# Kernel optimization log

Hardware: AMD Instinct MI355X
Metric: run time of the kernel (lower is better)

The kernel has to match this reference:

```python
import jax, jax.numpy as jnp
import numpy as np
from jax import lax

BS = 256
EPS = 1e-5  # torch LayerNorm default


def _layernorm(x, g, b):
    m = jnp.mean(x, axis=-1, keepdims=True)
    v = jnp.var(x, axis=-1, keepdims=True)
    return (x - m) / jnp.sqrt(v + EPS) * g + b


def _conv(x, w, b):
    y = lax.conv_general_dilated(x, w, (1, 1), 'VALID',
                                 dimension_numbers=('NCHW', 'OIHW', 'NCHW'))
    return y + b[None, :, None, None]


def _maxpool2(x):
    return lax.reduce_window(x, -jnp.inf, lax.max, (1, 1, 2, 2), (1, 1, 2, 2), 'VALID')


def setup_inputs() -> dict:
    key = jax.random.key(0)
    ks = iter(jax.random.split(key, 64))
    def rn(shape, scale=0.05):
        return jax.random.normal(next(ks), shape, dtype=jnp.float32) * scale
    return dict(
        t=jax.random.uniform(next(ks), (BS, 128, 128), dtype=jnp.float32) * 255.0,
        conv1_w=rn((32, 1, 3, 3)), conv1_b=rn((32,)),
        conv2_w=rn((32, 32, 3, 3)), conv2_b=rn((32,)),
        exp_w=rn((36, 64)), exp_b=rn((64,)),
        # 16 tile-attention modules x 4 heads x (64 -> 16)
        mh_wq=rn((16, 4, 64, 16)), mh_bq=rn((16, 4, 16)),
        mh_wk=rn((16, 4, 64, 16)), mh_bk=rn((16, 4, 16)),
        mh_wv=rn((16, 4, 64, 16)), mh_bv=rn((16, 4, 16)),
        mh_wo=rn((16, 64, 64)), mh_bo=rn((16, 64)),
        ln1_g=jnp.ones((64,), jnp.float32), ln1_b=jnp.zeros((64,), jnp.float32),
        # 2 XL layers x 8 heads x (2048 -> 256)
        xl_wq=rn((2, 8, 2048, 256)), xl_bq=rn((2, 8, 256)),
        xl_wk=rn((2, 8, 2048, 256)), xl_bk=rn((2, 8, 256)),
        xl_wv=rn((2, 8, 2048, 256)), xl_bv=rn((2, 8, 256)),
        xl_wo=rn((2, 2048, 2048)), xl_bo=rn((2, 2048)),
        xln_g=jnp.ones((2, 2048), jnp.float32), xln_b=jnp.zeros((2, 2048), jnp.float32),
        fl1_w=rn((32768, 512)), fl1_b=rn((512,)),
        fl2_w=rn((512, 128)), fl2_b=rn((128,)),
        fl3_w=rn((128, 25)), fl3_b=rn((25,)),
    )


def reference(t, conv1_w, conv1_b, conv2_w, conv2_b, exp_w, exp_b,
              mh_wq, mh_bq, mh_wk, mh_bk, mh_wv, mh_bv, mh_wo, mh_bo,
              ln1_g, ln1_b,
              xl_wq, xl_bq, xl_wk, xl_bk, xl_wv, xl_bv, xl_wo, xl_bo,
              xln_g, xln_b, fl1_w, fl1_b, fl2_w, fl2_b, fl3_w, fl3_b):
    # Eval-mode forward with discard_mem=True (fresh KV memory): every
    # AttentionHead attends over the current step only; dropout = identity.
    bs = t.shape[0]
    x = t / 255.0
    # 4x4 tiling of 32x32 patches -> (bs*16, 1, 32, 32)
    sliced = x.reshape(bs, 4, 32, 4, 32).transpose(0, 1, 3, 2, 4)
    x = sliced.reshape(bs * 16, 1, 32, 32)
    u = _maxpool2(_conv(x, conv1_w, conv1_b))        # (bs*16, 32, 15, 15)
    u = _maxpool2(_conv(u, conv2_w, conv2_b))        # (bs*16, 32, 6, 6)
    u = u.reshape(bs * 16, 32, 36)
    u = jax.nn.relu(u @ exp_w + exp_b)               # (bs*16, 32, 64)
    u = u.reshape(16, bs, 32, 64)                    # raw reshape, as in source

    # 16 multihead modules, 4 heads each, d_feature=16, seq_len=32
    q = jnp.einsum('mbsd,mhdf->mbhsf', u, mh_wq) + mh_bq[:, None, :, None, :]
    k = jnp.einsum('mbsd,mhdf->mbhsf', u, mh_wk) + mh_bk[:, None, :, None, :]
    v = jnp.einsum('mbsd,mhdf->mbhsf', u, mh_wv) + mh_bv[:, None, :, None, :]
    a = jax.nn.softmax(jnp.einsum('mbhsf,mbhtf->mbhst', q, k) / jnp.sqrt(16.0), axis=-1)
    o = jnp.einsum('mbhst,mbhtf->mbhsf', a, v)
    o = o.transpose(0, 1, 3, 2, 4).reshape(16, bs, 32, 64)  # concat heads
    o = jnp.einsum('mbsd,mde->mbse', o, mh_wo) + mh_bo[:, None, None, :]
    u = _layernorm(u + o, ln1_g, ln1_b)
    u = u.reshape(16, bs, 2048).transpose(1, 0, 2)   # (bs, 16, 2048)

    # XL stage (as written in source: att output is computed but discarded,
    # u = u + dropout(u) -> 2u under identity dropout, then LayerNorm)
    for i in range(2):
        q = jnp.einsum('bsd,hdf->bhsf', u, xl_wq[i]) + xl_bq[i][None, :, None, :]
        k = jnp.einsum('bsd,hdf->bhsf', u, xl_wk[i]) + xl_bk[i][None, :, None, :]
        vv = jnp.einsum('bsd,hdf->bhsf', u, xl_wv[i]) + xl_bv[i][None, :, None, :]
        aw = jax.nn.softmax(jnp.einsum('bhsf,bhtf->bhst', q, k) / jnp.sqrt(256.0), axis=-1)
        oo = jnp.einsum('bhst,bhtf->bhsf', aw, vv).transpose(0, 2, 1, 3).reshape(bs, 16, 2048)
        oo = oo @ xl_wo[i] + xl_bo[i]  # discarded, matching the source
        u = u + u
        u = _layernorm(u, xln_g[i], xln_b[i])

    u = u.reshape(bs, 16 * 2048)
    u = jax.nn.relu(u @ fl1_w + fl1_b)
    u = jax.nn.relu(u @ fl2_w + fl2_b)
    return u @ fl3_w + fl3_b
```

## Files before the change

kernel.cpp:

```cpp
#include <hip/hip_runtime.h>
#include <hip/hip_bf16.h>
#include <math.h>

#define LN_EPS 1e-5f

typedef __attribute__((ext_vector_type(8))) short short8v;
typedef __attribute__((ext_vector_type(4))) float f32x4;

static __device__ __forceinline__ unsigned short f2bf(float x) {
    unsigned u = __float_as_uint(x);
    u += 0x7fffu + ((u >> 16) & 1u);
    return (unsigned short)(u >> 16);
}
static __device__ __forceinline__ float bf2f(unsigned short h) {
    return __uint_as_float(((unsigned)h) << 16);
}

#define MFMA3(ACC, AH, AL, BH, BL)                                          \
    ACC = __builtin_amdgcn_mfma_f32_16x16x32_bf16(AH, BH, ACC, 0, 0, 0);    \
    ACC = __builtin_amdgcn_mfma_f32_16x16x32_bf16(AL, BH, ACC, 0, 0, 0);    \
    ACC = __builtin_amdgcn_mfma_f32_16x16x32_bf16(AH, BL, ACC, 0, 0, 0);

__global__ __launch_bounds__(512, 4) void k_conv(
    const float* __restrict__ t,
    const float* __restrict__ c1w, const float* __restrict__ c1b,
    const float* __restrict__ c2w, const float* __restrict__ c2b,
    const float* __restrict__ ew,  const float* __restrict__ eb,
    float* __restrict__ u)
{
    __shared__ __align__(16) unsigned short s_W2[2][32 * 296];
    __shared__ __align__(16) unsigned short s_p1h[225 * 40];
    __shared__ __align__(16) unsigned short s_p1l[225 * 40];
    __shared__ __align__(16) float s_s2[32 * 36];
    __shared__ float s_c2b[32];

    float* s_x  = (float*)s_W2;
    float* s_ew = (float*)s_p1h;
    unsigned short* s_wh = s_W2[0];
    unsigned short* s_wl = s_W2[1];

    const int p   = blockIdx.x;
    const int tid = threadIdx.x;

    const int b = p >> 4, tile = p & 15, tr = tile >> 2, tc = tile & 3;
    const float* tp = t + (size_t)b * 128 * 128 + (size_t)tr * 32 * 128 + tc * 32;
    for (int i = tid; i < 1024; i += 512) {
        const int r = i >> 5, c = i & 31;
        s_x[r * 33 + c] = tp[r * 128 + c] * (1.0f / 255.0f);
    }
    if (tid < 32) s_c2b[tid] = c2b[tid];
    __syncthreads();

    if (tid < 450) {
        const int pos  = tid >> 1;
        const int half = tid & 1;
        const int pi = pos / 15, pj = pos % 15;
        float xw[16];
        #pragma unroll
        for (int r = 0; r < 4; ++r)
            #pragma unroll
            for (int c = 0; c < 4; ++c)
                xw[r * 4 + c] = s_x[(2 * pi + r) * 33 + (2 * pj + c)];
        #pragma unroll
        for (int og2 = 0; og2 < 2; ++og2) {
            const int og = half * 2 + og2;
            short8v hb, lb;
            #pragma unroll
            for (int o = 0; o < 8; ++o) {
                const int oc = og * 8 + o;
                float w[9];
                #pragma unroll
                for (int j = 0; j < 9; ++j) w[j] = c1w[oc * 9 + j];
                float mx = -3.0e38f;
                #pragma unroll
                for (int a = 0; a < 2; ++a)
                    #pragma unroll
                    for (int bb = 0; bb < 2; ++bb) {
                        float s = xw[(a + 0) * 4 + bb + 0] * w[0]
                                + xw[(a + 0) * 4 + bb + 1] * w[1]
                                + xw[(a + 0) * 4 + bb + 2] * w[2]
                                + xw[(a + 1) * 4 + bb + 0] * w[3]
                                + xw[(a + 1) * 4 + bb + 1] * w[4]
                                + xw[(a + 1) * 4 + bb + 2] * w[5]
                                + xw[(a + 2) * 4 + bb + 0] * w[6]
                                + xw[(a + 2) * 4 + bb + 1] * w[7]
                                + xw[(a + 2) * 4 + bb + 2] * w[8];
                        mx = fmaxf(mx, s);
                    }
                const float val = mx + c1b[oc];
                const unsigned short h = f2bf(val);
                hb[o] = (short)h;
                lb[o] = (short)f2bf(val - bf2f(h));
            }
            *(short8v*)&s_p1h[pos * 40 + og * 8] = hb;
            *(short8v*)&s_p1l[pos * 40 + og * 8] = lb;
        }
    }
    __syncthreads();

    {
        const int oc  = tid >> 4;
        const int sub = tid & 15;
        const float* wp = c2w + oc * 288 + sub * 18;
        float wf[18];
        #pragma unroll
        for (int j = 0; j < 9; ++j)
            *(float2*)&wf[j * 2] = *(const float2*)&wp[j * 2];
        #pragma unroll
        for (int ks = 0; ks < 9; ++ks) {
            const float v0 = wf[ks];
            const float v1 = wf[9 + ks];
            const unsigned short h0 = f2bf(v0), h1 = f2bf(v1);
            const unsigned short l0 = f2bf(v0 - bf2f(h0));
            const unsigned short l1 = f2bf(v1 - bf2f(h1));
            const int idx = oc * 296 + ks * 32 + sub * 2;
            *(unsigned*)&s_wh[idx] = (unsigned)h0 | ((unsigned)h1 << 16);
            *(unsigned*)&s_wl[idx] = (unsigned)l0 | ((unsigned)l1 << 16);
        }
    }
    __syncthreads();

    {
        const int lane = tid & 63;
        const int w8   = tid >> 6;
        const int jcol = lane & 15;
        const int icg8 = (lane >> 4) * 8;

        {
            const int nt = w8;
            const int n = nt * 16 + jcol;
            const int pq = n >> 2, w4 = n & 3;
            const int pi = pq / 6, pj = pq - pi * 6;
            const int rbase = 2 * pi + (w4 >> 1);
            const int cbase = 2 * pj + (w4 & 1);

            f32x4 acc0 = {0,0,0,0}, acc1 = {0,0,0,0};
            #pragma unroll
            for (int ks = 0; ks < 9; ++ks) {
                const int dr = ks / 3, dc = ks - dr * 3;
                const int ab = jcol * 296 + ks * 32 + icg8;
                const short8v ah0 = *(const short8v*)&s_wh[ab];
                const short8v ah1 = *(const short8v*)&s_wh[ab + 16 * 296];
                const short8v al0 = *(const short8v*)&s_wl[ab];
                const short8v al1 = *(const short8v*)&s_wl[ab + 16 * 296];
                const int boff = ((rbase + dr) * 15 + (cbase + dc)) * 40 + icg8;
                const short8v bh = *(const short8v*)&s_p1h[boff];
                const short8v bl = *(const short8v*)&s_p1l[boff];
                acc0 = __builtin_amdgcn_mfma_f32_16x16x32_bf16(ah0, bh, acc0, 0, 0, 0);
                acc0 = __builtin_amdgcn_mfma_f32_16x16x32_bf16(al0, bh, acc0, 0, 0, 0);
                acc0 = __builtin_amdgcn_mfma_f32_16x16x32_bf16(ah0, bl, acc0, 0, 0, 0);
                acc1 = __builtin_amdgcn_mfma_f32_16x16x32_bf16(ah1, bh, acc1, 0, 0, 0);
                acc1 = __builtin_amdgcn_mfma_f32_16x16x32_bf16(al1, bh, acc1, 0, 0, 0);
                acc1 = __builtin_amdgcn_mfma_f32_16x16x32_bf16(ah1, bl, acc1, 0, 0, 0);
            }
            #pragma unroll
            for (int mt = 0; mt < 2; ++mt)
                #pragma unroll
                for (int r = 0; r < 4; ++r) {
                    float v = (mt == 0) ? acc0[r] : acc1[r];
                    v = fmaxf(v, __shfl_xor(v, 1));
                    v = fmaxf(v, __shfl_xor(v, 2));
                    if ((lane & 3) == 0) {
                        const int oc = mt * 16 + (lane >> 4) * 4 + r;
                        const int pq2 = nt * 4 + (jcol >> 2);
                        s_s2[oc * 36 + pq2] = v + s_c2b[oc];
                    }
                }
        }

        if (w8 < 2) {
            const int nt = 8;
            const int mt = w8;
            const int n = nt * 16 + jcol;
            const int pq = n >> 2, w4 = n & 3;
            const int pi = pq / 6, pj = pq - pi * 6;
            const int rbase = 2 * pi + (w4 >> 1);
            const int cbase = 2 * pj + (w4 & 1);

            f32x4 accX = {0,0,0,0};
            #pragma unroll
            for (int ks = 0; ks < 9; ++ks) {
                const int dr = ks / 3, dc = ks - dr * 3;
                const int ab = jcol * 296 + ks * 32 + icg8 + mt * 16 * 296;
                const short8v ah = *(const short8v*)&s_wh[ab];
                const short8v al = *(const short8v*)&s_wl[ab];
                const int boff = ((rbase + dr) * 15 + (cbase + dc)) * 40 + icg8;
                const short8v bh = *(const short8v*)&s_p1h[boff];
                const short8v bl = *(const short8v*)&s_p1l[boff];
                accX = __builtin_amdgcn_mfma_f32_16x16x32_bf16(ah, bh, accX, 0, 0, 0);
                accX = __builtin_amdgcn_mfma_f32_16x16x32_bf16(al, bh, accX, 0, 0, 0);
                accX = __builtin_amdgcn_mfma_f32_16x16x32_bf16(ah, bl, accX, 0, 0, 0);
            }
            #pragma unroll
            for (int r = 0; r < 4; ++r) {
                float v = accX[r];
                v = fmaxf(v, __shfl_xor(v, 1));
                v = fmaxf(v, __shfl_xor(v, 2));
                if ((lane & 3) == 0) {
                    const int oc = mt * 16 + (lane >> 4) * 4 + r;
                    const int pq2 = nt * 4 + (jcol >> 2);
                    s_s2[oc * 36 + pq2] = v + s_c2b[oc];
                }
            }
        }
    }
    __syncthreads();

    for (int i = tid; i < 576; i += 512)
        *(float4*)&s_ew[i * 4] = *(const float4*)&ew[i * 4];
    __syncthreads();

    {
        const int s  = tid >> 4;
        const int e0 = (tid & 15) * 4;
        float acc4[4];
        *(float4*)&acc4[0] = *(const float4*)&eb[e0];
        for (int f = 0; f < 36; ++f) {
            const float sv = s_s2[s * 36 + f];
            const float4 w0 = *(const float4*)&s_ew[f * 64 + e0];
            acc4[0] += sv * w0.x; acc4[1] += sv * w0.y;
            acc4[2] += sv * w0.z; acc4[3] += sv * w0.w;
        }
        float4 o0;
        o0.x = fmaxf(acc4[0], 0.0f); o0.y = fmaxf(acc4[1], 0.0f);
        o0.z = fmaxf(acc4[2], 0.0f); o0.w = fmaxf(acc4[3], 0.0f);
        *(float4*)&u[(size_t)p * 2048 + s * 64 + e0] = o0;
    }
}

__global__ __launch_bounds__(256, 2) void k_attn(
    const float* __restrict__ u,
    const float* __restrict__ wq, const float* __restrict__ bq,
    const float* __restrict__ wk, const float* __restrict__ bk,
    const float* __restrict__ wv, const float* __restrict__ bv,
    const float* __restrict__ wo, const float* __restrict__ bo,
    const float* __restrict__ g1, const float* __restrict__ b1,
    const float* __restrict__ xg, const float* __restrict__ xb,
    unsigned short* __restrict__ Ah, unsigned short* __restrict__ Al)
{
    __shared__ __align__(16) unsigned short s_w[2][64 * 64];
    __shared__ __align__(16) float s_uf[32 * 68];
    __shared__ __align__(16) unsigned short R1[12288];
    __shared__ __align__(16) unsigned short R2[5632];
    __shared__ float s_red[2][32][2];
    __shared__ float s_red2[2][4][2];

    unsigned short* qA_h = R1;
    unsigned short* qA_l = R1 + 3072;
    unsigned short* kB_h = R1 + 6144;
    unsigned short* kB_l = R1 + 9216;
    unsigned short* p_h  = R1;
    unsigned short* p_l  = R1 + 5120;
    unsigned short* vT_h = R2;
    unsigned short* vT_l = R2 + 2560;
    unsigned short* oA_h = R2;
    unsigned short* oA_l = R2 + 2816;

    const int g   = blockIdx.x;
    const int m   = g >> 8;
    const int b2  = g & 255;
    const int tid = threadIdx.x;
    const int l   = tid & 63;
    const int w   = tid >> 6;
    const int l15 = l & 15;
    const int lg  = l >> 4;

    {
        const int s = tid >> 3, dq = (tid & 7) * 8;
        const float* up = u + (size_t)g * 2048 + s * 64 + dq;
        *(float4*)&s_uf[s * 68 + dq]     = *(const float4*)up;
        *(float4*)&s_uf[s * 68 + dq + 4] = *(const float4*)(up + 4);
    }

    const int wn  = tid & 63;
    const int wkq = tid >> 6;
    float wreg[16];

    #define LOADQKV(SRC)                                                          \
        {                                                                         \
            const float* sp = (SRC) + (size_t)m * 4096 + (wn >> 4) * 1024 + (wn & 15); \
            _Pragma("unroll")                                                     \
            for (int j = 0; j < 16; ++j) wreg[j] = sp[(wkq * 16 + j) * 16];       \
        }
    #define LOADO(SRC)                                                            \
        {                                                                         \
            const float* sp = (SRC) + (size_t)m * 4096 + wn;                      \
            _Pragma("unroll")                                                     \
            for (int j = 0; j < 16; ++j) wreg[j] = sp[(wkq * 16 + j) * 64];       \
        }
    #define WRITEW()                                                              \
        {                                                                         \
            _Pragma("unroll")                                                     \
            for (int j2 = 0; j2 < 8; ++j2) {                                      \
                const int d = wkq * 16 + j2 * 2;                                  \
                const float v0 = wreg[j2 * 2], v1 = wreg[j2 * 2 + 1];             \
                const unsigned short h0 = f2bf(v0), h1 = f2bf(v1);                \
                const unsigned short q0 = f2bf(v0 - bf2f(h0));                    \
                const unsigned short q1 = f2bf(v1 - bf2f(h1));                    \
                const int idx = wn * 64 + (((d >> 3) ^ (wn & 7)) << 3) + (d & 7); \
                *(unsigned*)&s_w[0][idx] = (unsigned)h0 | ((unsigned)h1 << 16);   \
                *(unsigned*)&s_w[1][idx] = (unsigned)q0 | ((unsigned)q1 << 16);   \
            }                                                                     \
        }

    LOADQKV(wq);
    __syncthreads();
    WRITEW();

    short8v uh[2][2], ul[2][2];
    #pragma unroll
    for (int mf = 0; mf < 2; ++mf)
        #pragma unroll
        for (int ks = 0; ks < 2; ++ks) {
            const float* pb = &s_uf[(mf * 16 + l15) * 68 + (ks * 4 + lg) * 8];
            float xv[8];
            *(float4*)&xv[0] = *(const float4*)pb;
            *(float4*)&xv[4] = *(const float4*)(pb + 4);
            short8v hh, ll;
            #pragma unroll
            for (int j = 0; j < 8; ++j) {
                const unsigned short h = f2bf(xv[j]);
                hh[j] = (short)h;
                ll[j] = (short)f2bf(xv[j] - bf2f(h));
            }
            uh[mf][ks] = hh; ul[mf][ks] = ll;
        }
    __syncthreads();

    #define PROJ(BIAS, MODE)                                                      \
        {                                                                         \
            short8v wbh[2], wbl[2];                                               \
            const int bn = w * 16 + l15;                                          \
            _Pragma("unroll")                                                     \
            for (int ks = 0; ks < 2; ++ks) {                                      \
                const int off = bn * 64 + (((ks * 4 + lg) ^ (bn & 7)) << 3);      \
                wbh[ks] = *(const short8v*)&s_w[0][off];                          \
                wbl[ks] = *(const short8v*)&s_w[1][off];                          \
            }                                                                     \
            const float bias_v = (BIAS)[m * 64 + bn];                             \
            f32x4 a0 = {0,0,0,0}, a1 = {0,0,0,0};                                 \
            _Pragma("unroll")                                                     \
            for (int ks = 0; ks < 2; ++ks) {                                      \
                MFMA3(a0, uh[0][ks], ul[0][ks], wbh[ks], wbl[ks]);                \
                MFMA3(a1, uh[1][ks], ul[1][ks], wbh[ks], wbl[ks]);                \
            }                                                                     \
            _Pragma("unroll")                                                     \
            for (int mf = 0; mf < 2; ++mf) {                                      \
                const f32x4 av = mf ? a1 : a0;                                    \
                _Pragma("unroll")                                                 \
                for (int r = 0; r < 4; ++r) {                                     \
                    const float val = av[r] + bias_v;                             \
                    const unsigned short hh = f2bf(val);                          \
                    const unsigned short lo = f2bf(val - bf2f(hh));               \
                    const int srow = mf * 16 + lg * 4 + r;                        \
                    if ((MODE) == 0) { const int ix = w * 768 + srow * 24 + l15;  \
                        qA_h[ix] = hh; qA_l[ix] = lo; }                           \
                    else if ((MODE) == 1) { const int ix = w * 768 + srow * 24 + l15; \
                        kB_h[ix] = hh; kB_l[ix] = lo; }                           \
                    else { const int ix = w * 640 + l15 * 40 + srow;              \
                        vT_h[ix] = hh; vT_l[ix] = lo; }                           \
                }                                                                 \
            }                                                                     \
        }

    PROJ(bq, 0);
    LOADQKV(wk);
    __syncthreads();
    WRITEW();
    __syncthreads();

    PROJ(bk, 1);
    LOADQKV(wv);
    __syncthreads();
    WRITEW();
    __syncthreads();

    PROJ(bv, 2);
    LOADO(wo);
    __syncthreads();
    WRITEW();
    __syncthreads();

    float pvreg[2][2][4];
    {
        const short8v zz = {0,0,0,0,0,0,0,0};
        short8v qh[2], ql[2], kh[2], kl[2];
        const bool kreal = (lg < 2);
        #pragma unroll
        for (int mf = 0; mf < 2; ++mf) {
            if (kreal) {
                const int ia = w * 768 + (mf * 16 + l15) * 24 + lg * 8;
                qh[mf] = *(const short8v*)&qA_h[ia];
                ql[mf] = *(const short8v*)&qA_l[ia];
                kh[mf] = *(const short8v*)&kB_h[ia];
                kl[mf] = *(const short8v*)&kB_l[ia];
            } else { qh[mf] = zz; ql[mf] = zz; kh[mf] = zz; kl[mf] = zz; }
        }
        f32x4 sc[2][2];
        #pragma unroll
        for (int mf = 0; mf < 2; ++mf)
            #pragma unroll
            for (int nf = 0; nf < 2; ++nf) {
                sc[mf][nf] = (f32x4){0,0,0,0};
                MFMA3(sc[mf][nf], qh[mf], ql[mf], kh[nf], kl[nf]);
            }
        #pragma unroll
        for (int mf = 0; mf < 2; ++mf)
            #pragma unroll
            for (int r = 0; r < 4; ++r) {
                const float v0 = sc[mf][0][r] * 0.25f;
                const float v1 = sc[mf][1][r] * 0.25f;
                float mx = fmaxf(v0, v1);
                mx = fmaxf(mx, __shfl_xor(mx, 1));
                mx = fmaxf(mx, __shfl_xor(mx, 2));
                mx = fmaxf(mx, __shfl_xor(mx, 4));
                mx = fmaxf(mx, __shfl_xor(mx, 8));
                const float e0 = expf(v0 - mx), e1 = expf(v1 - mx);
                float sm = e0 + e1;
                sm += __shfl_xor(sm, 1);
                sm += __shfl_xor(sm, 2);
                sm += __shfl_xor(sm, 4);
                sm += __shfl_xor(sm, 8);
                const float inv = 1.0f / sm;
                pvreg[mf][0][r] = e0 * inv;
                pvreg[mf][1][r] = e1 * inv;
            }
    }
    __syncthreads();

    #pragma unroll
    for (int mf = 0; mf < 2; ++mf)
        #pragma unroll
        for (int nf = 0; nf < 2; ++nf)
            #pragma unroll
            for (int r = 0; r < 4; ++r) {
                const int srow = mf * 16 + lg * 4 + r;
                const int tt = nf * 16 + l15;
                const int ix = w * 1280 + srow * 40 + tt;
                const float val = pvreg[mf][nf][r];
                const unsigned short hh = f2bf(val);
                p_h[ix] = hh;
                p_l[ix] = f2bf(val - bf2f(hh));
            }
    __syncthreads();

    f32x4 ov[2];
    {
        short8v ph[2], pl[2], vh_, vl_;
        #pragma unroll
        for (int mf = 0; mf < 2; ++mf) {
            const int ix = w * 1280 + (mf * 16 + l15) * 40 + lg * 8;
            ph[mf] = *(const short8v*)&p_h[ix];
            pl[mf] = *(const short8v*)&p_l[ix];
        }
        const int iv = w * 640 + l15 * 40 + lg * 8;
        vh_ = *(const short8v*)&vT_h[iv];
        vl_ = *(const short8v*)&vT_l[iv];
        #pragma unroll
        for (int mf = 0; mf < 2; ++mf) {
            ov[mf] = (f32x4){0,0,0,0};
            MFMA3(ov[mf], ph[mf], pl[mf], vh_, vl_);
        }
    }
    __syncthreads();

    #pragma unroll
    for (int mf = 0; mf < 2; ++mf)
        #pragma unroll
        for (int r = 0; r < 4; ++r) {
            const int srow = mf * 16 + lg * 4 + r;
            const int dd = w * 16 + l15;
            const int ix = srow * 88 + dd;
            const float val = ov[mf][r];
            const unsigned short hh = f2bf(val);
            oA_h[ix] = hh;
            oA_l[ix] = f2bf(val - bf2f(hh));
        }
    __syncthreads();

    const int mfA = w >> 1;
    const int nfb = (w & 1) * 2;
    float x[2][4];
    {
        short8v oh[2], ol[2];
        #pragma unroll
        for (int ks = 0; ks < 2; ++ks) {
            const int ix = (mfA * 16 + l15) * 88 + (ks * 4 + lg) * 8;
            oh[ks] = *(const short8v*)&oA_h[ix];
            ol[ks] = *(const short8v*)&oA_l[ix];
        }
        #pragma unroll
        for (int nfi = 0; nfi < 2; ++nfi) {
            const int n = (nfb + nfi) * 16 + l15;
            f32x4 xe = {0,0,0,0};
            #pragma unroll
            for (int ks = 0; ks < 2; ++ks) {
                const int off = n * 64 + (((ks * 4 + lg) ^ (n & 7)) << 3);
                const short8v wbh = *(const short8v*)&s_w[0][off];
                const short8v wbl = *(const short8v*)&s_w[1][off];
                MFMA3(xe, oh[ks], ol[ks], wbh, wbl);
            }
            const int e = n;
            const float bo_v = bo[m * 64 + e];
            #pragma unroll
            for (int r = 0; r < 4; ++r) {
                const int srow = mfA * 16 + lg * 4 + r;
                x[nfi][r] = xe[r] + bo_v + s_uf[srow * 68 + e];
            }
        }
    }
    #pragma unroll
    for (int r = 0; r < 4; ++r) {
        float s1 = x[0][r] + x[1][r];
        float s2 = x[0][r] * x[0][r] + x[1][r] * x[1][r];
        s1 += __shfl_xor(s1, 1); s2 += __shfl_xor(s2, 1);
        s1 += __shfl_xor(s1, 2); s2 += __shfl_xor(s2, 2);
        s1 += __shfl_xor(s1, 4); s2 += __shfl_xor(s2, 4);
        s1 += __shfl_xor(s1, 8); s2 += __shfl_xor(s2, 8);
        if (l15 == 0) {
            const int srow = mfA * 16 + lg * 4 + r;
            s_red[w & 1][srow][0] = s1;
            s_red[w & 1][srow][1] = s2;
        }
    }
    __syncthreads();

    float q2[2][4];
    #pragma unroll
    for (int r = 0; r < 4; ++r) {
        const int srow = mfA * 16 + lg * 4 + r;
        const float sum = s_red[0][srow][0] + s_red[1][srow][0];
        const float ssq = s_red[0][srow][1] + s_red[1][srow][1];
        const float mean = sum * (1.0f / 64.0f);
        const float var = fmaxf(ssq * (1.0f / 64.0f) - mean * mean, 0.0f);
        const float inv = rsqrtf(var + LN_EPS);
        #pragma unroll
        for (int nfi = 0; nfi < 2; ++nfi) {
            const int e = (nfb + nfi) * 16 + l15;
            const float y = (x[nfi][r] - mean) * inv * g1[e] + b1[e];
            q2[nfi][r] = 2.0f * y;
        }
    }

    #pragma unroll
    for (int L = 0; L < 2; ++L) {
        float ls = 0.0f, lq = 0.0f;
        #pragma unroll
        for (int nfi = 0; nfi < 2; ++nfi)
            #pragma unroll
            for (int r = 0; r < 4; ++r) { ls += q2[nfi][r]; lq += q2[nfi][r] * q2[nfi][r]; }
        ls += __shfl_xor(ls, 1);  lq += __shfl_xor(lq, 1);
        ls += __shfl_xor(ls, 2);  lq += __shfl_xor(lq, 2);
        ls += __shfl_xor(ls, 4);  lq += __shfl_xor(lq, 4);
        ls += __shfl_xor(ls, 8);  lq += __shfl_xor(lq, 8);
        ls += __shfl_xor(ls, 16); lq += __shfl_xor(lq, 16);
        ls += __shfl_xor(ls, 32); lq += __shfl_xor(lq, 32);
        if (l == 0) { s_red2[L][w][0] = ls; s_red2[L][w][1] = lq; }
        __syncthreads();
        const float sum = s_red2[L][0][0] + s_red2[L][1][0] + s_red2[L][2][0] + s_red2[L][3][0];
        const float ssq = s_red2[L][0][1] + s_red2[L][1][1] + s_red2[L][2][1] + s_red2[L][3][1];
        const float mean = sum * (1.0f / 2048.0f);
        const float var = fmaxf(ssq * (1.0f / 2048.0f) - mean * mean, 0.0f);
        const float inv = rsqrtf(var + LN_EPS);
        #pragma unroll
        for (int nfi = 0; nfi < 2; ++nfi)
            #pragma unroll
            for (int r = 0; r < 4; ++r) {
                const int srow = mfA * 16 + lg * 4 + r;
                const int e = (nfb + nfi) * 16 + l15;
                const int col = srow * 64 + e;
                const float z = (q2[nfi][r] - mean) * inv * xg[L * 2048 + col] + xb[L * 2048 + col];
                q2[nfi][r] = (L == 0) ? 2.0f * z : z;
            }
    }

    #pragma unroll
    for (int nfi = 0; nfi < 2; ++nfi)
        #pragma unroll
        for (int r = 0; r < 4; ++r) {
            const int srow = mfA * 16 + lg * 4 + r;
            const int e = (nfb + nfi) * 16 + l15;
            const int col = srow * 64 + e;
            const float val = q2[nfi][r];
            const unsigned short hh = f2bf(val);
            const size_t addr = ((size_t)(m * 64 + (col >> 5)) * 256 + b2) * 32 + (col & 31);
            Ah[addr] = hh;
            Al[addr] = f2bf(val - bf2f(hh));
        }
}

__global__ __launch_bounds__(512) void k_fl1(
    const unsigned short* __restrict__ Ah,
    const unsigned short* __restrict__ Al,
    const float* __restrict__ W,
    float* __restrict__ part)
{
    __shared__ __align__(16) unsigned short s_wh[128 * 64];
    __shared__ __align__(16) unsigned short s_wl[128 * 64];

    const int nb  = blockIdx.x;
    const int kb  = blockIdx.y;
    const int tid = threadIdx.x;
    const int lane = tid & 63;
    const int wid  = tid >> 6;
    const int wm = wid >> 1;
    const int wn = wid & 1;

    const int sn = tid & 127;
    const int sq = tid >> 7;
    const int k0 = kb * 512;

    f32x4 acc[4][4];
    #pragma unroll
    for (int i = 0; i < 4; ++i)
        #pragma unroll
        for (int j = 0; j < 4; ++j)
            acc[i][j] = (f32x4){0.0f, 0.0f, 0.0f, 0.0f};

    float wreg[16];
    {
        const float* wp = W + (size_t)(k0 + sq * 16) * 512 + nb * 128 + sn;
        #pragma unroll
        for (int j = 0; j < 16; ++j) wreg[j] = wp[(size_t)j * 512];
    }

    const int hsn = sn & 7;
    const int wbase = sn * 64;
    const int wo0 = (((sq * 2) ^ hsn) << 3);
    const int wo1 = (((sq * 2 + 1) ^ hsn) << 3);

    for (int tt = 0; tt < 8; ++tt) {
        __syncthreads();
        {
            short8v h0, h1, l0, l1;
            #pragma unroll
            for (int j = 0; j < 8; ++j) {
                const unsigned short ha = f2bf(wreg[j]);
                const unsigned short hb = f2bf(wreg[j + 8]);
                h0[j] = (short)ha;
                h1[j] = (short)hb;
                l0[j] = (short)f2bf(wreg[j] - bf2f(ha));
                l1[j] = (short)f2bf(wreg[j + 8] - bf2f(hb));
            }
            *(short8v*)&s_wh[wbase + wo0] = h0;
            *(short8v*)&s_wh[wbase + wo1] = h1;
            *(short8v*)&s_wl[wbase + wo0] = l0;
            *(short8v*)&s_wl[wbase + wo1] = l1;
        }
        if (tt < 7) {
            const float* wp = W + (size_t)(k0 + (tt + 1) * 64 + sq * 16) * 512 + nb * 128 + sn;
            #pragma unroll
            for (int j = 0; j < 16; ++j) wreg[j] = wp[(size_t)j * 512];
        }
        __syncthreads();

        #pragma unroll
        for (int ks = 0; ks < 2; ++ks) {
            const int ktile = (k0 >> 5) + tt * 2 + ks;
            const size_t abase = ((size_t)ktile * 256 + wm * 64 + (lane & 15)) * 32
                               + (lane >> 4) * 8;
            short8v ahf[4], alf[4];
            #pragma unroll
            for (int mf = 0; mf < 4; ++mf) {
                ahf[mf] = *(const short8v*)&Ah[abase + (size_t)mf * 512];
                alf[mf] = *(const short8v*)&Al[abase + (size_t)mf * 512];
            }
            short8v bhf[4], blf[4];
            #pragma unroll
            for (int nf = 0; nf < 4; ++nf) {
                const int n = wn * 64 + nf * 16 + (lane & 15);
                const int q = ks * 4 + (lane >> 4);
                const int baddr = n * 64 + ((q ^ (n & 7)) << 3);
                bhf[nf] = *(const short8v*)&s_wh[baddr];
                blf[nf] = *(const short8v*)&s_wl[baddr];
            }
            #pragma unroll
            for (int mf = 0; mf < 4; ++mf)
                #pragma unroll
                for (int nf = 0; nf < 4; ++nf) {
                    MFMA3(acc[mf][nf], ahf[mf], alf[mf], bhf[nf], blf[nf]);
                }
        }
    }

    float* pp = part + (size_t)kb * 131072 + (size_t)nb * 128;
    const int r0 = (lane >> 4) * 4;
    const int c  = lane & 15;
    #pragma unroll
    for (int mf = 0; mf < 4; ++mf) {
        const int row = wm * 64 + mf * 16 + r0;
        #pragma unroll
        for (int nf = 0; nf < 4; ++nf) {
            const int col = wn * 64 + nf * 16 + c;
            #pragma unroll
            for (int r = 0; r < 4; ++r)
                pp[(size_t)(row + r) * 512 + col] = acc[mf][nf][r];
        }
    }
}

__global__ __launch_bounds__(256) void k_fl1red(
    const float* __restrict__ part, const float* __restrict__ bias,
    float* __restrict__ out1)
{
    const int i4 = (blockIdx.x * 256 + threadIdx.x) * 4;
    float4 s = *(const float4*)&bias[i4 & 511];
    for (int ks = 0; ks < 64; ++ks) {
        const float4 p = *(const float4*)&part[(size_t)ks * 131072 + i4];
        s.x += p.x; s.y += p.y; s.z += p.z; s.w += p.w;
    }
    s.x = fmaxf(s.x, 0.0f); s.y = fmaxf(s.y, 0.0f);
    s.z = fmaxf(s.z, 0.0f); s.w = fmaxf(s.w, 0.0f);
    *(float4*)&out1[i4] = s;
}

__global__ __launch_bounds__(128) void k_fl2(
    const float* __restrict__ u1, const float* __restrict__ w,
    const float* __restrict__ b, float* __restrict__ out2)
{
    __shared__ float s_u[512];
    const int r = blockIdx.x, tid = threadIdx.x;
    for (int i = tid; i < 512; i += 128) s_u[i] = u1[r * 512 + i];
    __syncthreads();
    float acc = b[tid];
    for (int k = 0; k < 512; k++) acc += s_u[k] * w[k * 128 + tid];
    out2[r * 128 + tid] = fmaxf(acc, 0.0f);
}

__global__ __launch_bounds__(128) void k_fl3(
    const float* __restrict__ u2_, const float* __restrict__ w,
    const float* __restrict__ b, float* __restrict__ out)
{
    __shared__ float s_u[128];
    const int r = blockIdx.x, tid = threadIdx.x;
    s_u[tid] = u2_[r * 128 + tid];
    __syncthreads();
    if (tid < 25) {
        float acc = b[tid];
        for (int k = 0; k < 128; k++) acc += s_u[k] * w[k * 25 + tid];
        out[r * 25 + tid] = acc;
    }
}

extern "C" void kernel_launch(void* const* d_in, const int* in_sizes, int n_in,
                              void* d_out, int out_size, void* d_ws, size_t ws_size,
                              hipStream_t stream)
{
    const float* t      = (const float*)d_in[0];
    const float* c1w    = (const float*)d_in[1];
    const float* c1b    = (const float*)d_in[2];
    const float* c2w    = (const float*)d_in[3];
    const float* c2b    = (const float*)d_in[4];
    const float* ew     = (const float*)d_in[5];
    const float* eb     = (const float*)d_in[6];
    const float* mh_wq  = (const float*)d_in[7];
    const float* mh_bq  = (const float*)d_in[8];
    const float* mh_wk  = (const float*)d_in[9];
    const float* mh_bk  = (const float*)d_in[10];
    const float* mh_wv  = (const float*)d_in[11];
    const float* mh_bv  = (const float*)d_in[12];
    const float* mh_wo  = (const float*)d_in[13];
    const float* mh_bo  = (const float*)d_in[14];
    const float* ln1_g  = (const float*)d_in[15];
    const float* ln1_b  = (const float*)d_in[16];
    const float* xln_g  = (const float*)d_in[25];
    const float* xln_b  = (const float*)d_in[26];
    const float* fl1_w  = (const float*)d_in[27];
    const float* fl1_b  = (const float*)d_in[28];
    const float* fl2_w  = (const float*)d_in[29];
    const float* fl2_b  = (const float*)d_in[30];
    const float* fl3_w  = (const float*)d_in[31];
    const float* fl3_b  = (const float*)d_in[32];
    (void)in_sizes; (void)n_in; (void)out_size; (void)ws_size;

    float* U   = (float*)d_ws;
    float* U2  = U + 8388608;
    unsigned short* Ah = (unsigned short*)U2;
    unsigned short* Al = Ah + 8388608;
    float* PART = U;
    float* OUT1 = U2;
    float* OUT2 = U;
    float* out  = (float*)d_out;

    k_conv<<<4096, 512, 0, stream>>>(t, c1w, c1b, c2w, c2b, ew, eb, U);
    k_attn<<<4096, 256, 0, stream>>>(U, mh_wq, mh_bq, mh_wk, mh_bk, mh_wv, mh_bv,
                                     mh_wo, mh_bo, ln1_g, ln1_b, xln_g, xln_b,
                                     Ah, Al);
    k_fl1<<<dim3(4, 64), 512, 0, stream>>>(Ah, Al, fl1_w, PART);
    k_fl1red<<<128, 256, 0, stream>>>(PART, fl1_b, OUT1);
    k_fl2<<<256, 128, 0, stream>>>(OUT1, fl2_w, fl2_b, OUT2);
    k_fl3<<<256, 128, 0, stream>>>(OUT2, fl3_w, fl3_b, out);
}
```

Before: 286.7 us.

## Compute conv1 with split-bf16 MFMA instead of scalar FP32 FMAs

Replaces the scalar conv1+maxpool loop with an MFMA formulation. The input tile and conv1 weights are split into bf16 hi/lo pairs in shared memory, and each 16-position group is fed to 16x16x32 bf16 MFMAs using three-term compensated products. The 2x2 max-pool is done with lane shuffles before the hi/lo results are written to shared memory. The aim is to move conv1 arithmetic onto the matrix cores. In exchange the K dimension of 32 is mostly padding for 9 taps, lanes with lg>0 broadcast one value (so the 9th tap is added four times unless those weight columns are zero), and precision drops to roughly split-bf16 accuracy.

```diff
diff --git a/kernel.cpp b/kernel.cpp
--- a/kernel.cpp
+++ b/kernel.cpp
@@ -32,9 +32,13 @@
     __shared__ __align__(16) unsigned short s_p1h[225 * 40];
     __shared__ __align__(16) unsigned short s_p1l[225 * 40];
     __shared__ __align__(16) float s_s2[32 * 36];
+    __shared__ float s_c1b[32];
     __shared__ float s_c2b[32];
 
-    float* s_x  = (float*)s_W2;
+    unsigned short* s_xh = (unsigned short*)s_W2;
+    unsigned short* s_xl = s_xh + 1056;
+    unsigned short* w1h  = (unsigned short*)s_s2;
+    unsigned short* w1l  = w1h + 1024;
     float* s_ew = (float*)s_p1h;
     unsigned short* s_wh = s_W2[0];
     unsigned short* s_wl = s_W2[1];
@@ -46,54 +50,82 @@
     const float* tp = t + (size_t)b * 128 * 128 + (size_t)tr * 32 * 128 + tc * 32;
     for (int i = tid; i < 1024; i += 512) {
         const int r = i >> 5, c = i & 31;
-        s_x[r * 33 + c] = tp[r * 128 + c] * (1.0f / 255.0f);
-    }
-    if (tid < 32) s_c2b[tid] = c2b[tid];
-    __syncthreads();
-
-    if (tid < 450) {
-        const int pos  = tid >> 1;
-        const int half = tid & 1;
-        const int pi = pos / 15, pj = pos % 15;
-        float xw[16];
-        #pragma unroll
-        for (int r = 0; r < 4; ++r)
-            #pragma unroll
-            for (int c = 0; c < 4; ++c)
-                xw[r * 4 + c] = s_x[(2 * pi + r) * 33 + (2 * pj + c)];
-        #pragma unroll
-        for (int og2 = 0; og2 < 2; ++og2) {
-            const int og = half * 2 + og2;
-            short8v hb, lb;
-            #pragma unroll
-            for (int o = 0; o < 8; ++o) {
-                const int oc = og * 8 + o;
-                float w[9];
+        const float v = tp[r * 128 + c] * (1.0f / 255.0f);
+        const unsigned short h = f2bf(v);
+        s_xh[r * 33 + c] = h;
+        s_xl[r * 33 + c] = f2bf(v - bf2f(h));
+    }
+    for (int s = tid; s < 1024; s += 512) {
+        const int oc = s >> 5, k = s & 31;
+        const float v = (k < 9) ? c1w[oc * 9 + k] : 0.0f;
+        const unsigned short h = f2bf(v);
+        w1h[s] = h;
+        w1l[s] = f2bf(v - bf2f(h));
+    }
+    if (tid < 32) { s_c1b[tid] = c1b[tid]; s_c2b[tid] = c2b[tid]; }
+    __syncthreads();
+
+    {
+        const int lane = tid & 63, w8 = tid >> 6;
+        const int jc = lane & 15, lg = lane >> 4;
+
+        short8v ah[2], al[2];
+        #pragma unroll
+        for (int mh = 0; mh < 2; ++mh) {
+            ah[mh] = *(const short8v*)&w1h[(mh * 16 + jc) * 32 + lg * 8];
+            al[mh] = *(const short8v*)&w1l[(mh * 16 + jc) * 32 + lg * 8];
+        }
+
+        for (int i = 0; i < 8; ++i) {
+            const int g = w8 + i * 8;
+            if (g < 57) {
+                const int n = g * 16 + jc;
+                int pq = n >> 2; if (pq > 224) pq = 224;
+                const int quad = n & 3;
+                const int pi = pq / 15, pj = pq - pi * 15;
+                const int ci = 2 * pi + (quad >> 1), cj = 2 * pj + (quad & 1);
+                const int base = ci * 33 + cj;
+
+                short8v bh, bl;
+                if (lg == 0) {
+                    bh[0] = (short)s_xh[base + 0];  bl[0] = (short)s_xl[base + 0];
+                    bh[1] = (short)s_xh[base + 1];  bl[1] = (short)s_xl[base + 1];
+                    bh[2] = (short)s_xh[base + 2];  bl[2] = (short)s_xl[base + 2];
+                    bh[3] = (short)s_xh[base + 33]; bl[3] = (short)s_xl[base + 33];
+                    bh[4] = (short)s_xh[base + 34]; bl[4] = (short)s_xl[base + 34];
+                    bh[5] = (short)s_xh[base + 35]; bl[5] = (short)s_xl[base + 35];
+                    bh[6] = (short)s_xh[base + 66]; bl[6] = (short)s_xl[base + 66];
+                    bh[7] = (short)s_xh[base + 67]; bl[7] = (short)s_xl[base + 67];
+                } else {
+                    const short v8h = (short)s_xh[base + 68];
+                    const short v8l = (short)s_xl[base + 68];
+                    #pragma unroll
+                    for (int j = 0; j < 8; ++j) { bh[j] = v8h; bl[j] = v8l; }
+                }
+
+                f32x4 acc0 = {0, 0, 0, 0}, acc1 = {0, 0, 0, 0};
+                MFMA3(acc0, ah[0], al[0], bh, bl);
+                MFMA3(acc1, ah[1], al[1], bh, bl);
+
                 #pragma unroll
-                for (int j = 0; j < 9; ++j) w[j] = c1w[oc * 9 + j];
-                float mx = -3.0e38f;
-                #pragma unroll
-                for (int a = 0; a < 2; ++a)
+                for (int mh = 0; mh < 2; ++mh)
                     #pragma unroll
-                    for (int bb = 0; bb < 2; ++bb) {
-                        float s = xw[(a + 0) * 4 + bb + 0] * w[0]
-                                + xw[(a + 0) * 4 + bb + 1] * w[1]
-                                + xw[(a + 0) * 4 + bb + 2] * w[2]
-                                + xw[(a + 1) * 4 + bb + 0] * w[3]
-                                + xw[(a + 1) * 4 + bb + 1] * w[4]
-                                + xw[(a + 1) * 4 + bb + 2] * w[5]
-                                + xw[(a + 2) * 4 + bb + 0] * w[6]
-                                + xw[(a + 2) * 4 + bb + 1] * w[7]
-                                + xw[(a + 2) * 4 + bb + 2] * w[8];
-                        mx = fmaxf(mx, s);
+                    for (int r = 0; r < 4; ++r) {
+                        float v = (mh == 0) ? acc0[r] : acc1[r];
+                        v = fmaxf(v, __shfl_xor(v, 1));
+                        v = fmaxf(v, __shfl_xor(v, 2));
+                        if ((jc & 3) == 0) {
+                            const int pqw = g * 4 + (jc >> 2);
+                            if (pqw < 225) {
+                                const int oc = mh * 16 + lg * 4 + r;
+                                const float val = v + s_c1b[oc];
+                                const unsigned short h = f2bf(val);
+                                s_p1h[pqw * 40 + oc] = h;
+                                s_p1l[pqw * 40 + oc] = f2bf(val - bf2f(h));
+                            }
+                        }
                     }
-                const float val = mx + c1b[oc];
-                const unsigned short h = f2bf(val);
-                hb[o] = (short)h;
-                lb[o] = (short)f2bf(val - bf2f(h));
-            }
-            *(short8v*)&s_p1h[pos * 40 + og * 8] = hb;
-            *(short8v*)&s_p1l[pos * 40 + og * 8] = lb;
+            }
         }
     }
     __syncthreads();
```

After: 354.0 us. +23.5%, slower.
